# Performance work log

Measured on AMD Instinct MI355X. Metric: run time of the kernel, lower is better.

## Reference

```python
import jax, jax.numpy as jnp
import numpy as np

D_MODEL = 512
NHEAD = 8
SEQ = 2048
BATCH = 4


def setup_inputs() -> dict:
    key = jax.random.key(0)
    ks = jax.random.split(key, 6)
    s = 0.02
    return {
        "x": jax.random.normal(ks[0], (SEQ, BATCH, D_MODEL), jnp.float32),
        "w_in_g": jax.random.normal(ks[1], (3 * D_MODEL, D_MODEL), jnp.float32) * s,
        "b_in_g": jnp.zeros((3 * D_MODEL,), jnp.float32),
        "w_out_g": jax.random.normal(ks[2], (D_MODEL, D_MODEL), jnp.float32) * s,
        "b_out_g": jnp.zeros((D_MODEL,), jnp.float32),
        "w_in_l": jax.random.normal(ks[3], (3 * D_MODEL, D_MODEL), jnp.float32) * s,
        "b_in_l": jnp.zeros((3 * D_MODEL,), jnp.float32),
        "w_out_l": jax.random.normal(ks[4], (D_MODEL, D_MODEL), jnp.float32) * s,
        "b_out_l": jnp.zeros((D_MODEL,), jnp.float32),
        "local_window_size": 128,
    }


def _mha(x, w_in, b_in, w_out, b_out, nhead):
    # x: (S, B, D); faithful to torch nn.MultiheadAttention (batch_first=False)
    S, B, D = x.shape
    dh = D // nhead
    qkv = x @ w_in.T + b_in                       # (S, B, 3D)
    q, k, v = jnp.split(qkv, 3, axis=-1)
    q = q.reshape(S, B, nhead, dh)
    k = k.reshape(S, B, nhead, dh)
    v = v.reshape(S, B, nhead, dh)
    scores = jnp.einsum("sbhd,tbhd->bhst", q, k) / jnp.sqrt(jnp.float32(dh))
    attn = jax.nn.softmax(scores, axis=-1)        # (B, H, S, S)
    out = jnp.einsum("bhst,tbhd->sbhd", attn, v).reshape(S, B, D)
    return out @ w_out.T + b_out


def reference(x, w_in_g, b_in_g, w_out_g, b_out_g,
              w_in_l, b_in_l, w_out_l, b_out_l, local_window_size):
    S, B, D = x.shape
    W = int(local_window_size)
    global_out = _mha(x, w_in_g, b_in_g, w_out_g, b_out_g, NHEAD)
    # Non-overlapping local windows tile the sequence (S % W == 0 here),
    # so the per-window loop == window-batched attention.
    nW = S // W
    xw = x.reshape(nW, W, B, D).transpose(1, 0, 2, 3).reshape(W, nW * B, D)
    lw = _mha(xw, w_in_l, b_in_l, w_out_l, b_out_l, NHEAD)
    local_out = lw.reshape(W, nW, B, D).transpose(1, 0, 2, 3).reshape(S, B, D)
    return global_out + local_out
```

## Files before the change

### kernel.cpp

```cpp
#include <hip/hip_runtime.h>
#include <hip/hip_bf16.h>
#include <stdint.h>

typedef __attribute__((ext_vector_type(8))) short bf16x8;
typedef __attribute__((ext_vector_type(8))) unsigned short u16x8;
typedef __attribute__((ext_vector_type(4))) float f32x4;
typedef __attribute__((ext_vector_type(16))) float f32x16;

#define DEV __device__ __forceinline__

DEV f32x4 mfma16(bf16x8 a, bf16x8 b, f32x4 c) {
  return __builtin_amdgcn_mfma_f32_16x16x32_bf16(a, b, c, 0, 0, 0);
}

DEV f32x16 mfma32(bf16x8 a, bf16x8 b, f32x16 c) {
  return __builtin_amdgcn_mfma_f32_32x32x16_bf16(a, b, c, 0, 0, 0);
}

DEV void gload_lds16(const void* g, void* l) {
  __builtin_amdgcn_global_load_lds(
      (__attribute__((address_space(1))) void*)(g),
      (__attribute__((address_space(3))) void*)(l), 16, 0, 0);
}

DEV unsigned short f2bf(float f) {
  __hip_bfloat16 h = __float2bfloat16(f);
  return __builtin_bit_cast(unsigned short, h);
}

__global__ __launch_bounds__(256) void convert_all(
    const float4* __restrict__ s0, const float4* __restrict__ s1,
    const float4* __restrict__ s2, const float4* __restrict__ s3,
    const float4* __restrict__ s4, ushort4* __restrict__ dst)
{
  const int n0 = 1048576, n1 = 196608, n3 = 65536;
  int i = blockIdx.x * 256 + threadIdx.x;
  const float4* s; int off;
  if (i < n0)                 { s = s0; off = 0; }
  else if (i < n0 + n1)       { s = s1; off = n0; }
  else if (i < n0 + 2*n1)     { s = s2; off = n0 + n1; }
  else if (i < n0 + 2*n1+n3)  { s = s3; off = n0 + 2*n1; }
  else                        { s = s4; off = n0 + 2*n1 + n3; }
  float4 v = s[i - off];
  ushort4 o;
  o.x = f2bf(v.x); o.y = f2bf(v.y); o.z = f2bf(v.z); o.w = f2bf(v.w);
  dst[i] = o;
}

#define GEMM_STAGE(Ap, Wp, k0v, bufi)                                          \
  {                                                                            \
    _Pragma("unroll")                                                          \
    for (int is = 0; is < 2; ++is) {                                           \
      const int row = is*64 + (t >> 3);                                        \
      const int slot = (t & 7) ^ (row & 7);                                    \
      gload_lds16((Ap) + (long)(m0 + row)*K + (k0v) + slot*8,                  \
                  (char*)&As[bufi][0] + (is*512 + t)*16);                      \
      gload_lds16((Wp) + (long)(n0 + row)*K + (k0v) + slot*8,                  \
                  (char*)&Ws[bufi][0] + (is*512 + t)*16);                      \
    }                                                                          \
  }

#define GEMM_COMPUTE(cur, NJ, WCMUL)                                           \
  {                                                                            \
    const char* Apl = (const char*)&As[cur][0];                                \
    const char* Wpl = (const char*)&Ws[cur][0];                                \
    __builtin_amdgcn_s_setprio(1);                                             \
    _Pragma("unroll")                                                          \
    for (int kk = 0; kk < 2; ++kk) {                                           \
      bf16x8 af[4], wf[NJ];                                                    \
      _Pragma("unroll")                                                        \
      for (int i = 0; i < 4; ++i) {                                            \
        const int row = wr*64 + i*16 + l16;                                    \
        const int slot = (kk*4 + g16) ^ (row & 7);                             \
        af[i] = *(const bf16x8*)(Apl + row*128 + slot*16);                     \
      }                                                                        \
      _Pragma("unroll")                                                        \
      for (int j = 0; j < NJ; ++j) {                                           \
        const int row = wc*WCMUL + j*16 + l16;                                 \
        const int slot = (kk*4 + g16) ^ (row & 7);                             \
        wf[j] = *(const bf16x8*)(Wpl + row*128 + slot*16);                     \
      }                                                                        \
      _Pragma("unroll")                                                        \
      for (int i = 0; i < 4; ++i)                                              \
        _Pragma("unroll")                                                      \
        for (int j = 0; j < NJ; ++j)                                           \
          acc[i][j] = mfma16(af[i], wf[j], acc[i][j]);                         \
    }                                                                          \
    __builtin_amdgcn_s_setprio(0);                                             \
  }

__global__ __launch_bounds__(512) void gemm_qkv(
    const __hip_bfloat16* __restrict__ A0,
    const __hip_bfloat16* __restrict__ Wg, const float* __restrict__ bg,
    const __hip_bfloat16* __restrict__ Wl, const float* __restrict__ bl,
    __hip_bfloat16* __restrict__ qkg, __hip_bfloat16* __restrict__ vtg,
    __hip_bfloat16* __restrict__ qkl, __hip_bfloat16* __restrict__ vtl,
    int M, int N, int K)
{
  __shared__ __attribute__((aligned(16))) char SMEM[65536];
  __hip_bfloat16 (*As)[8192] = (__hip_bfloat16(*)[8192])SMEM;
  __hip_bfloat16 (*Ws)[8192] = (__hip_bfloat16(*)[8192])(SMEM + 32768);
  const int t = threadIdx.x;
  const int lane = t & 63, wid = t >> 6;
  const int g16 = lane >> 4, l16 = lane & 15;
  const int wr = wid >> 2, wc = wid & 3;
  const int bid = blockIdx.x;
  const int xcd = bid & 7, seq = bid >> 3;
  const int sel = xcd >= 4;
  const int xh = xcd & 3;
  const int m0 = (xh*16 + (seq & 15)) * 128;
  const int n0 = (seq >> 4) * 128;
  const __hip_bfloat16* W0 = sel ? Wl : Wg;
  const float* b0 = sel ? bl : bg;
  __hip_bfloat16* qkp = sel ? qkl : qkg;
  __hip_bfloat16* vtp = sel ? vtl : vtg;

  f32x4 acc[4][2] = {};
  const int nks = K >> 6;

  GEMM_STAGE(A0, W0, 0, 0)
  for (int step = 0; step < nks; ++step) {
    const int cur = step & 1;
    if (step + 1 < nks) {
      GEMM_STAGE(A0, W0, (step+1) << 6, cur ^ 1)
      asm volatile("s_waitcnt vmcnt(4)" ::: "memory");
    } else {
      asm volatile("s_waitcnt vmcnt(0)" ::: "memory");
    }
    __builtin_amdgcn_s_barrier();
    asm volatile("" ::: "memory");
    GEMM_COMPUTE(cur, 2, 32)
    asm volatile("" ::: "memory");
    __builtin_amdgcn_s_barrier();
  }

  if (n0 < 1024) {
#pragma unroll
    for (int i = 0; i < 4; ++i) {
      const int gr = m0 + wr*64 + i*16 + g16*4;
#pragma unroll
      for (int j = 0; j < 2; ++j) {
        const int gc = n0 + wc*32 + j*16 + l16;
        const float bias = b0[gc];
        const float scl = (gc >= 512) ? 0.180336880f : 1.0f;
#pragma unroll
        for (int r = 0; r < 4; ++r)
          qkp[(long)(gr + r)*1024 + gc] =
              __float2bfloat16((acc[i][j][r] + bias) * scl);
      }
    }
  } else {
    const int n0l = n0 - 1024;
    short* T = (short*)SMEM;
#pragma unroll
    for (int i = 0; i < 4; ++i) {
      const int sl = wr*16 + i*4 + g16;
#pragma unroll
      for (int j = 0; j < 2; ++j) {
        const int gcl = wc*32 + j*16 + l16;
        const float bias = b0[n0 + gcl];
#pragma unroll
        for (int r = 0; r < 4; ++r)
          T[gcl*136 + r*32 + sl] = (short)f2bf(acc[i][j][r] + bias);
      }
    }
    __syncthreads();
    const int d = t & 127, b4 = t >> 7;
    __hip_bfloat16* dst = vtp + ((long)(b4*512 + n0l + d))*2048 + (m0 >> 2);
#pragma unroll
    for (int k = 0; k < 4; ++k) {
      u16x8 v = *(const u16x8*)(T + d*136 + b4*32 + k*8);
      *(u16x8*)(dst + k*8) = v;
    }
  }
}

__global__ __launch_bounds__(512) void gemm_out(
    const __hip_bfloat16* __restrict__ A0, const __hip_bfloat16* __restrict__ W0,
    const float* __restrict__ b0,
    const __hip_bfloat16* __restrict__ A1, const __hip_bfloat16* __restrict__ W1,
    const float* __restrict__ b1,
    float* __restrict__ Cout, int M, int N, int K)
{
  __shared__ __attribute__((aligned(16))) __hip_bfloat16 As[2][128*64];
  __shared__ __attribute__((aligned(16))) __hip_bfloat16 Ws[2][64*64];
  const int t = threadIdx.x;
  const int lane = t & 63, wid = t >> 6;
  const int g16 = lane >> 4, l16 = lane & 15;
  const int wr = wid >> 2, wc = wid & 3;
  const int bid = blockIdx.x;
  const int xcd = bid & 7, pos = bid >> 3;
  const int m0 = (xcd*8 + (pos & 7)) * 128, n0 = (pos >> 3) * 64;

  f32x4 acc[4][1] = {};
  const int nks = K >> 6;
  const int NS = 2*nks;

#define OUT_STAGE(Ap, Wp, k0v, bufi)                                           \
  {                                                                            \
    _Pragma("unroll")                                                          \
    for (int is = 0; is < 2; ++is) {                                           \
      const int row = is*64 + (t >> 3);                                        \
      const int slot = (t & 7) ^ (row & 7);                                    \
      gload_lds16((Ap) + (long)(m0 + row)*K + (k0v) + slot*8,                  \
                  (char*)&As[bufi][0] + (is*512 + t)*16);                      \
    }                                                                          \
    {                                                                          \
      const int row = t >> 3;                                                  \
      const int slot = (t & 7) ^ (row & 7);                                    \
      gload_lds16((Wp) + (long)(n0 + row)*K + (k0v) + slot*8,                  \
                  (char*)&Ws[bufi][0] + t*16);                                 \
    }                                                                          \
  }

  OUT_STAGE(A0, W0, 0, 0)
  for (int step = 0; step < NS; ++step) {
    const int cur = step & 1;
    if (step + 1 < NS) {
      const int nstep = step + 1;
      const __hip_bfloat16* Ap = (nstep >= nks) ? A1 : A0;
      const __hip_bfloat16* Wp = (nstep >= nks) ? W1 : W0;
      const int k0 = ((nstep >= nks) ? (nstep - nks) : nstep) << 6;
      OUT_STAGE(Ap, Wp, k0, cur ^ 1)
      asm volatile("s_waitcnt vmcnt(3)" ::: "memory");
    } else {
      asm volatile("s_waitcnt vmcnt(0)" ::: "memory");
    }
    __builtin_amdgcn_s_barrier();
    asm volatile("" ::: "memory");
    GEMM_COMPUTE(cur, 1, 16)
    asm volatile("" ::: "memory");
    __builtin_amdgcn_s_barrier();
  }

#pragma unroll
  for (int i = 0; i < 4; ++i) {
    const int gr = m0 + wr*64 + i*16 + g16*4;
    const int gc = n0 + wc*16 + l16;
    const float bias = b0[gc] + b1[gc];
#pragma unroll
    for (int r = 0; r < 4; ++r)
      Cout[(long)(gr + r)*N + gc] = acc[i][0][r] + bias;
  }
}

__global__ __launch_bounds__(512) void flash_g256(
    const __hip_bfloat16* __restrict__ qk, const __hip_bfloat16* __restrict__ vt,
    __hip_bfloat16* __restrict__ outg, int S, int B)
{
  const int t = threadIdx.x, lane = t & 63, w = t >> 6;
  const int l32 = lane & 31, hf = lane >> 5;
  const int id = blockIdx.x;
  const int xcd = id & 7, seq = id >> 3;
  const int bh = xcd + 8*(seq & 3);
  const int qt = seq >> 2;
  const int b = bh >> 3, head = bh & 7;
  const int q0 = qt * 256;
  const int nkt = S >> 6;
  const int vtb = bh * 64;

  __shared__ __attribute__((aligned(16))) __hip_bfloat16 Kb[2][64*64];
  __shared__ __attribute__((aligned(16))) __hip_bfloat16 Vb[2][64*64];

  const int qw = q0 + w*32 + l32;
  bf16x8 qa[4];
  {
    const __hip_bfloat16* qp = qk + ((long)qw*B + b)*1024 + head*64 + hf*8;
#pragma unroll
    for (int ks = 0; ks < 4; ++ks)
      qa[ks] = *(const bf16x8*)(const void*)(qp + ks*16);
  }

  f32x16 oacc[2] = {};
  float lsum = 0.f;

#define GSTAGE(tile, bufi)                                                     \
  {                                                                            \
    const int kvs_ = (tile)*64;                                                \
    const int row_ = t >> 3;                                                   \
    const int sl_ = (t & 7) ^ (row_ & 7);                                      \
    gload_lds16(qk + ((long)(kvs_+row_)*B + b)*1024 + 512 + head*64 + sl_*8,   \
                (char*)&Kb[bufi][0] + t*16);                                   \
    gload_lds16(vt + (long)(vtb + row_)*2048 + kvs_ + sl_*8,                   \
                (char*)&Vb[bufi][0] + t*16);                                   \
  }

  GSTAGE(0, 0)

  for (int kt = 0; kt < nkt; ++kt) {
    const int cur = kt & 1;
    if (kt + 1 < nkt) {
      GSTAGE(kt + 1, cur ^ 1)
      asm volatile("s_waitcnt vmcnt(2)" ::: "memory");
    } else {
      asm volatile("s_waitcnt vmcnt(0)" ::: "memory");
    }
    __builtin_amdgcn_s_barrier();
    asm volatile("" ::: "memory");

    f32x16 sacc[2] = {};
    const char* Kp = (const char*)&Kb[cur][0];
    __builtin_amdgcn_s_setprio(1);
#pragma unroll
    for (int ks = 0; ks < 4; ++ks)
#pragma unroll
      for (int jb = 0; jb < 2; ++jb) {
        const int row = jb*32 + l32;
        const int slot = (ks*2 + hf) ^ (row & 7);
        bf16x8 kf = *(const bf16x8*)(Kp + row*128 + slot*16);
        sacc[jb] = mfma32(kf, qa[ks], sacc[jb]);
      }
    __builtin_amdgcn_s_setprio(0);

    unsigned pk[2][8];
#pragma unroll
    for (int jb = 0; jb < 2; ++jb)
#pragma unroll
      for (int rg = 0; rg < 4; ++rg)
#pragma unroll
        for (int hv = 0; hv < 2; ++hv) {
          const float p0 = __builtin_amdgcn_exp2f(sacc[jb][rg*4 + hv*2]);
          const float p1 = __builtin_amdgcn_exp2f(sacc[jb][rg*4 + hv*2 + 1]);
          lsum += p0 + p1;
          pk[jb][rg*2 + hv] =
              (unsigned)f2bf(p0) | ((unsigned)f2bf(p1) << 16);
        }

    const char* Vp = (const char*)&Vb[cur][0];
    __builtin_amdgcn_s_setprio(1);
#pragma unroll
    for (int ks = 0; ks < 4; ++ks) {
      const int q2 = ks & 1, jb = ks >> 1;
      unsigned w0 = pk[jb][4*q2 + 0], w2v = pk[jb][4*q2 + 2];
      asm volatile("v_permlane32_swap_b32 %0, %1" : "+v"(w0), "+v"(w2v));
      unsigned w1 = pk[jb][4*q2 + 1], w3v = pk[jb][4*q2 + 3];
      asm volatile("v_permlane32_swap_b32 %0, %1" : "+v"(w1), "+v"(w3v));
      union { unsigned u[4]; bf16x8 v; } pb;
      pb.u[0] = w0; pb.u[1] = w1; pb.u[2] = w2v; pb.u[3] = w3v;
#pragma unroll
      for (int db = 0; db < 2; ++db) {
        const int row = db*32 + l32;
        const int slot = (ks*2 + hf) ^ (row & 7);
        bf16x8 vf = *(const bf16x8*)(Vp + row*128 + slot*16);
        oacc[db] = mfma32(vf, pb.v, oacc[db]);
      }
    }
    __builtin_amdgcn_s_setprio(0);

    asm volatile("" ::: "memory");
    __builtin_amdgcn_s_barrier();
  }

  lsum += __shfl_xor(lsum, 32, 64);
  const float inv = 1.f / lsum;
  const long base = ((long)qw*B + b)*512 + head*64;
#pragma unroll
  for (int db = 0; db < 2; ++db)
#pragma unroll
    for (int rq = 0; rq < 4; ++rq) {
      ushort4 pkk;
      pkk.x = f2bf(oacc[db][rq*4 + 0]*inv);
      pkk.y = f2bf(oacc[db][rq*4 + 1]*inv);
      pkk.z = f2bf(oacc[db][rq*4 + 2]*inv);
      pkk.w = f2bf(oacc[db][rq*4 + 3]*inv);
      *(ushort4*)(outg + base + db*32 + rq*8 + hf*4) = pkk;
    }
}

__global__ __launch_bounds__(512) void flash_all(
    const __hip_bfloat16* __restrict__ qkg, const __hip_bfloat16* __restrict__ vtg,
    __hip_bfloat16* __restrict__ outg,
    const __hip_bfloat16* __restrict__ qkl, const __hip_bfloat16* __restrict__ vtl,
    __hip_bfloat16* __restrict__ outl,
    const int* __restrict__ wptr, int S, int B, int blkoff)
{
  const int t = threadIdx.x, lane = t & 63, w = t >> 6;
  const int g16 = lane >> 4, l16 = lane & 15;
  const int gid = blockIdx.x + blkoff;
  const int isl = gid >= 512;
  const int id = gid & 511;
  const __hip_bfloat16* qk = isl ? qkl : qkg;
  const __hip_bfloat16* vt = isl ? vtl : vtg;
  __hip_bfloat16* outb = isl ? outl : outg;
  const int Wn = isl ? wptr[0] : S;
  const int xcd = id & 7, seq = id >> 3;
  const int bh = xcd + 8*(seq & 3);
  const int qt = seq >> 2;
  const int b = bh >> 3, h = bh & 7;
  const int q0 = qt * 128;
  const int kv0 = (q0 / Wn) * Wn;
  const int nkt = Wn >> 6;
  const int vtb = bh * 64;

  __shared__ __attribute__((aligned(16))) __hip_bfloat16 Kb[2][64*64];
  __shared__ __attribute__((aligned(16))) __hip_bfloat16 Vb[2][64*64];
  __shared__ __attribute__((aligned(16))) short Pl[8][16*72];

  const int qrow = q0 + w*16 + l16;
  bf16x8 qa[2];
  {
    const __hip_bfloat16* qp = qk + ((long)qrow*B + b)*1024 + h*64 + g16*8;
    qa[0] = *(const bf16x8*)(const void*)qp;
    qa[1] = *(const bf16x8*)(const void*)(qp + 32);
  }
  bf16x8 aones;
#pragma unroll
  for (int e = 0; e < 8; ++e) aones[e] = (short)0x3F80;

  f32x4 o[4] = {};
  f32x4 ol = {};

#define STAGE(tile, bufi)                                                      \
  {                                                                            \
    const int kvs_ = kv0 + (tile)*64;                                          \
    const int row_ = t >> 3;                                                   \
    const int sl_ = (t & 7) ^ (row_ & 7);                                      \
    gload_lds16(qk + ((long)(kvs_+row_)*B + b)*1024 + 512 + h*64 + sl_*8,      \
                (char*)&Kb[bufi][0] + t*16);                                   \
    gload_lds16(vt + (long)(vtb + row_)*2048 + kvs_ + sl_*8,                   \
                (char*)&Vb[bufi][0] + t*16);                                   \
  }

  STAGE(0, 0)

  for (int kt = 0; kt < nkt; ++kt) {
    const int cur = kt & 1;
    if (kt + 1 < nkt) {
      STAGE(kt + 1, cur ^ 1)
      asm volatile("s_waitcnt vmcnt(2)" ::: "memory");
    } else {
      asm volatile("s_waitcnt vmcnt(0)" ::: "memory");
    }
    __builtin_amdgcn_s_barrier();
    asm volatile("" ::: "memory");

    f32x4 s[4] = {};
    const char* Kp = (const char*)&Kb[cur][0];
    __builtin_amdgcn_s_setprio(1);
#pragma unroll
    for (int kk = 0; kk < 2; ++kk)
#pragma unroll
      for (int j = 0; j < 4; ++j) {
        const int row = j*16 + l16;
        const int slot = (kk*4 + g16) ^ (row & 7);
        bf16x8 kf = *(const bf16x8*)(Kp + row*128 + slot*16);
        s[j] = mfma16(kf, qa[kk], s[j]);
      }
    __builtin_amdgcn_s_setprio(0);

    short* Pw = &Pl[w][0];
#pragma unroll
    for (int j = 0; j < 4; ++j) {
      short4 pk4;
      pk4.x = (short)f2bf(__builtin_amdgcn_exp2f(s[j][0]));
      pk4.y = (short)f2bf(__builtin_amdgcn_exp2f(s[j][1]));
      pk4.z = (short)f2bf(__builtin_amdgcn_exp2f(s[j][2]));
      pk4.w = (short)f2bf(__builtin_amdgcn_exp2f(s[j][3]));
      *(short4*)(Pw + l16*72 + j*16 + g16*4) = pk4;
    }

    __builtin_amdgcn_s_setprio(1);
#pragma unroll
    for (int kk = 0; kk < 2; ++kk) {
      bf16x8 pf = *(const bf16x8*)(Pw + l16*72 + kk*32 + g16*8);
      ol = mfma16(aones, pf, ol);
#pragma unroll
      for (int dblk = 0; dblk < 4; ++dblk) {
        const int row = dblk*16 + l16;
        const int slot = (kk*4 + g16) ^ (row & 7);
        bf16x8 vf = *(const bf16x8*)((const char*)&Vb[cur][0] + row*128 + slot*16);
        o[dblk] = mfma16(vf, pf, o[dblk]);
      }
    }
    __builtin_amdgcn_s_setprio(0);

    asm volatile("" ::: "memory");
    __builtin_amdgcn_s_barrier();
  }

  const float inv = 1.f / ol[0];
  const long obase = ((long)qrow*B + b)*512 + h*64;
#pragma unroll
  for (int dblk = 0; dblk < 4; ++dblk) {
    ushort4 pk;
    pk.x = f2bf(o[dblk][0]*inv); pk.y = f2bf(o[dblk][1]*inv);
    pk.z = f2bf(o[dblk][2]*inv); pk.w = f2bf(o[dblk][3]*inv);
    *(ushort4*)(outb + obase + dblk*16 + g16*4) = pk;
  }
}

extern "C" void kernel_launch(void* const* d_in, const int* in_sizes, int n_in,
                              void* d_out, int out_size, void* d_ws, size_t ws_size,
                              hipStream_t stream) {
  const float* x   = (const float*)d_in[0];
  const float* wig = (const float*)d_in[1];
  const float* big = (const float*)d_in[2];
  const float* wog = (const float*)d_in[3];
  const float* bog = (const float*)d_in[4];
  const float* wil = (const float*)d_in[5];
  const float* bil = (const float*)d_in[6];
  const float* wol = (const float*)d_in[7];
  const float* bol = (const float*)d_in[8];
  const int*   wsz = (const int*)d_in[9];

  char* ws = (char*)d_ws;
  __hip_bfloat16* xb    = (__hip_bfloat16*)(ws + 0);
  __hip_bfloat16* wigb  = (__hip_bfloat16*)(ws + 8388608);
  __hip_bfloat16* wilb  = (__hip_bfloat16*)(ws + 9961472);
  __hip_bfloat16* wogb  = (__hip_bfloat16*)(ws + 11534336);
  __hip_bfloat16* wolb  = (__hip_bfloat16*)(ws + 12058624);
  __hip_bfloat16* qkg   = (__hip_bfloat16*)(ws + 12582912);
  __hip_bfloat16* qkl   = (__hip_bfloat16*)(ws + 29360128);
  __hip_bfloat16* vtg   = (__hip_bfloat16*)(ws + 46137344);
  __hip_bfloat16* vtl   = (__hip_bfloat16*)(ws + 54525952);
  __hip_bfloat16* attng = xb;

  const int big_ws = ws_size >= (size_t)71303168;
  __hip_bfloat16* attnl = big_ws ? (__hip_bfloat16*)(ws + 62914560)
                                 : qkg;
  convert_all<<<6144, 256, 0, stream>>>(
      (const float4*)x, (const float4*)wig, (const float4*)wil,
      (const float4*)wog, (const float4*)wol, (ushort4*)ws);

  gemm_qkv<<<1536, 512, 0, stream>>>(xb, wigb, big, wilb, bil,
                                     qkg, vtg, qkl, vtl, 8192, 1536, 512);

  flash_g256<<<256, 512, 0, stream>>>(qkg, vtg, attng, 2048, 4);
  flash_all<<<512, 512, 0, stream>>>(qkg, vtg, attng, qkl, vtl, attnl,
                                     wsz, 2048, 4, 512);

  gemm_out<<<512, 512, 0, stream>>>(attng, wogb, bog, attnl, wolb, bol,
                                    (float*)d_out, 8192, 512, 512);
}
```

Before: 127.4 us.

## Split global attention KV range in half and add a combine kernel

The global flash kernel now launches twice as many blocks, each covering half of the key/value sequence. Each half writes its unnormalized bf16 output and row sums to scratch buffers. A new combine kernel adds the two halves and divides by the summed denominators. The local attention path becomes its own kernel. The goal is to fill more compute units during the global attention pass, at the cost of an extra launch, extra memory traffic, and bf16 rounding of unnormalized partial outputs.

```diff
diff --git a/kernel.cpp b/kernel.cpp
--- a/kernel.cpp
+++ b/kernel.cpp
@@ -26,6 +26,10 @@
 DEV unsigned short f2bf(float f) {
   __hip_bfloat16 h = __float2bfloat16(f);
   return __builtin_bit_cast(unsigned short, h);
+}
+
+DEV float bf2f(unsigned short u) {
+  return __builtin_bit_cast(float, (unsigned)u << 16);
 }
 
 __global__ __launch_bounds__(256) void convert_all(
@@ -246,17 +250,20 @@
 
 __global__ __launch_bounds__(512) void flash_g256(
     const __hip_bfloat16* __restrict__ qk, const __hip_bfloat16* __restrict__ vt,
-    __hip_bfloat16* __restrict__ outg, int S, int B)
+    __hip_bfloat16* __restrict__ oa, __hip_bfloat16* __restrict__ ob,
+    float* __restrict__ la, float* __restrict__ lb, int S, int B)
 {
   const int t = threadIdx.x, lane = t & 63, w = t >> 6;
   const int l32 = lane & 31, hf = lane >> 5;
-  const int id = blockIdx.x;
+  const int half = blockIdx.x >> 8;
+  const int id = blockIdx.x & 255;
   const int xcd = id & 7, seq = id >> 3;
   const int bh = xcd + 8*(seq & 3);
   const int qt = seq >> 2;
   const int b = bh >> 3, head = bh & 7;
   const int q0 = qt * 256;
-  const int nkt = S >> 6;
+  const int kv0 = half * (S >> 1);
+  const int nkt = S >> 7;
   const int vtb = bh * 64;
 
   __shared__ __attribute__((aligned(16))) __hip_bfloat16 Kb[2][64*64];
@@ -276,7 +283,7 @@
 
 #define GSTAGE(tile, bufi)                                                     \
   {                                                                            \
-    const int kvs_ = (tile)*64;                                                \
+    const int kvs_ = kv0 + (tile)*64;                                          \
     const int row_ = t >> 3;                                                   \
     const int sl_ = (t & 7) ^ (row_ & 7);                                      \
     gload_lds16(qk + ((long)(kvs_+row_)*B + b)*1024 + 512 + head*64 + sl_*8,   \
@@ -352,37 +359,50 @@
   }
 
   lsum += __shfl_xor(lsum, 32, 64);
-  const float inv = 1.f / lsum;
+  __hip_bfloat16* op = half ? ob : oa;
   const long base = ((long)qw*B + b)*512 + head*64;
 #pragma unroll
   for (int db = 0; db < 2; ++db)
 #pragma unroll
     for (int rq = 0; rq < 4; ++rq) {
       ushort4 pkk;
-      pkk.x = f2bf(oacc[db][rq*4 + 0]*inv);
-      pkk.y = f2bf(oacc[db][rq*4 + 1]*inv);
-      pkk.z = f2bf(oacc[db][rq*4 + 2]*inv);
-      pkk.w = f2bf(oacc[db][rq*4 + 3]*inv);
-      *(ushort4*)(outg + base + db*32 + rq*8 + hf*4) = pkk;
-    }
-}
-
-__global__ __launch_bounds__(512) void flash_all(
-    const __hip_bfloat16* __restrict__ qkg, const __hip_bfloat16* __restrict__ vtg,
-    __hip_bfloat16* __restrict__ outg,
-    const __hip_bfloat16* __restrict__ qkl, const __hip_bfloat16* __restrict__ vtl,
-    __hip_bfloat16* __restrict__ outl,
-    const int* __restrict__ wptr, int S, int B, int blkoff)
+      pkk.x = f2bf(oacc[db][rq*4 + 0]);
+      pkk.y = f2bf(oacc[db][rq*4 + 1]);
+      pkk.z = f2bf(oacc[db][rq*4 + 2]);
+      pkk.w = f2bf(oacc[db][rq*4 + 3]);
+      *(ushort4*)(op + base + db*32 + rq*8 + hf*4) = pkk;
+    }
+  if (hf == 0)
+    (half ? lb : la)[((long)qw*B + b)*8 + head] = lsum;
+}
+
+__global__ __launch_bounds__(256) void combine_halves(
+    const __hip_bfloat16* __restrict__ oa, const __hip_bfloat16* __restrict__ ob,
+    const float* __restrict__ la, const float* __restrict__ lb,
+    __hip_bfloat16* __restrict__ outg)
+{
+  const int i = blockIdx.x*256 + threadIdx.x;
+  const int row = i >> 6, c0 = (i & 63) << 3;
+  const int h = c0 >> 6;
+  const float inv = 1.f / (la[(long)row*8 + h] + lb[(long)row*8 + h]);
+  u16x8 a = *(const u16x8*)(oa + (long)row*512 + c0);
+  u16x8 bb = *(const u16x8*)(ob + (long)row*512 + c0);
+  u16x8 r;
+#pragma unroll
+  for (int e = 0; e < 8; ++e)
+    r[e] = f2bf((bf2f(a[e]) + bf2f(bb[e])) * inv);
+  *(u16x8*)(outg + (long)row*512 + c0) = r;
+}
+
+__global__ __launch_bounds__(512) void flash_local(
+    const __hip_bfloat16* __restrict__ qk, const __hip_bfloat16* __restrict__ vt,
+    __hip_bfloat16* __restrict__ outb, const int* __restrict__ wptr,
+    int S, int B)
 {
   const int t = threadIdx.x, lane = t & 63, w = t >> 6;
   const int g16 = lane >> 4, l16 = lane & 15;
-  const int gid = blockIdx.x + blkoff;
-  const int isl = gid >= 512;
-  const int id = gid & 511;
-  const __hip_bfloat16* qk = isl ? qkl : qkg;
-  const __hip_bfloat16* vt = isl ? vtl : vtg;
-  __hip_bfloat16* outb = isl ? outl : outg;
-  const int Wn = isl ? wptr[0] : S;
+  const int id = blockIdx.x;
+  const int Wn = wptr[0];
   const int xcd = id & 7, seq = id >> 3;
   const int bh = xcd + 8*(seq & 3);
   const int qt = seq >> 2;
@@ -513,11 +533,17 @@
   __hip_bfloat16* qkl   = (__hip_bfloat16*)(ws + 29360128);
   __hip_bfloat16* vtg   = (__hip_bfloat16*)(ws + 46137344);
   __hip_bfloat16* vtl   = (__hip_bfloat16*)(ws + 54525952);
+
+  __hip_bfloat16* oa    = xb;
+  __hip_bfloat16* ob    = (__hip_bfloat16*)d_out;
+  float*          la    = (float*)(ws + 8388608);
+  float*          lb    = (float*)(ws + 8650752);
   __hip_bfloat16* attng = xb;
 
   const int big_ws = ws_size >= (size_t)71303168;
   __hip_bfloat16* attnl = big_ws ? (__hip_bfloat16*)(ws + 62914560)
                                  : qkg;
+
   convert_all<<<6144, 256, 0, stream>>>(
       (const float4*)x, (const float4*)wig, (const float4*)wil,
       (const float4*)wog, (const float4*)wol, (ushort4*)ws);
@@ -525,9 +551,9 @@
   gemm_qkv<<<1536, 512, 0, stream>>>(xb, wigb, big, wilb, bil,
                                      qkg, vtg, qkl, vtl, 8192, 1536, 512);
 
-  flash_g256<<<256, 512, 0, stream>>>(qkg, vtg, attng, 2048, 4);
-  flash_all<<<512, 512, 0, stream>>>(qkg, vtg, attng, qkl, vtl, attnl,
-                                     wsz, 2048, 4, 512);
+  flash_g256<<<512, 512, 0, stream>>>(qkg, vtg, oa, ob, la, lb, 2048, 4);
+  flash_local<<<512, 512, 0, stream>>>(qkl, vtl, attnl, wsz, 2048, 4);
+  combine_halves<<<2048, 256, 0, stream>>>(oa, ob, la, lb, attng);
 
   gemm_out<<<512, 512, 0, stream>>>(attng, wogb, bog, attnl, wolb, bol,
                                     (float*)d_out, 8192, 512, 512);
```

New measurement: 125.9 us. Within noise of the previous version (-1.1%).
